# Optimization experiments

Measured on AMD Instinct MI355X. Metric: run time of the kernel, lower is better.

## Reference

```python
import jax, jax.numpy as jnp
import numpy as np

TAU = 5.0    # greybox_pars['ps'] residence time
DELTA = 1.0  # greybox_pars['Delta'] sample time


def setup_inputs() -> dict:
    key = jax.random.key(0)
    ks = jax.random.split(key, 8)
    B, T, Nx, Nu, H = 8192, 128, 3, 1, 64
    f32 = jnp.float32
    u = jax.random.normal(ks[0], (B, T, Nu), f32)
    x0 = jax.random.normal(ks[1], (B, Nx), f32)
    # fN MLP params: Dense(64, tanh) -> Dense(64, tanh) -> Dense(3)
    W1 = jax.random.normal(ks[2], (Nx + Nu, H), f32) / np.sqrt(Nx + Nu)
    b1 = jnp.zeros((H,), f32)
    W2 = jax.random.normal(ks[3], (H, H), f32) / np.sqrt(H)
    b2 = jnp.zeros((H,), f32)
    W3 = jax.random.normal(ks[4], (H, Nx), f32) / np.sqrt(H)
    b3 = jnp.zeros((Nx,), f32)
    # xuyscales
    xmean = jnp.array([1.0, 0.5, 0.3], f32)
    xstd = jnp.array([0.5, 0.2, 0.1], f32)
    umean = jnp.array([2.0], f32)
    ustd = jnp.array([0.5], f32)
    return dict(u=u, x0=x0, W1=W1, b1=b1, W2=W2, b2=b2, W3=W3, b3=b3,
                xmean=xmean, xstd=xstd, umean=umean, ustd=ustd)


def reference(u, x0, W1, b1, W2, b2, W3, b3, xmean, xstd, umean, ustd):
    def fnn(z):
        h = jnp.tanh(z @ W1 + b1)
        h = jnp.tanh(h @ W2 + b2)
        return h @ W3 + b3

    def fgreybox(x, uu):
        xp = x * xstd + xmean          # unscale state
        up = uu * ustd + umean         # unscale input
        Ca, Cb, Cc = xp[..., 0:1], xp[..., 1:2], xp[..., 2:3]
        Caf = up[..., 0:1]
        xdot = jnp.concatenate([(Caf - Ca) / TAU, -Cb / TAU, -Cc / TAU], axis=-1)
        return xdot / xstd

    def f(x, uu):
        return fgreybox(x, uu) + fnn(jnp.concatenate([x, uu], axis=-1))

    def step(x, ut):
        k1 = f(x, ut)
        k2 = f(x + DELTA * k1 / 2, ut)
        k3 = f(x + DELTA * k2 / 2, ut)
        k4 = f(x + DELTA * k3, ut)
        xplus = x + (DELTA / 6) * (k1 + 2 * k2 + 2 * k3 + k4)
        return xplus, x  # output y = current state (pre-update), as in the cell

    u_t = jnp.swapaxes(u, 0, 1)  # [T, B, Nu]
    _, ys = jax.lax.scan(step, x0, u_t)
    return jnp.swapaxes(ys, 0, 1)  # [B, T, Nx]
```

## Files before the change

### kernel.cpp

```cpp
#include <hip/hip_runtime.h>

typedef _Float16 f16x4 __attribute__((ext_vector_type(4)));
typedef _Float16 f16x8 __attribute__((ext_vector_type(8)));
typedef float    f32x4 __attribute__((ext_vector_type(4)));
typedef unsigned int u32x2 __attribute__((ext_vector_type(2)));

#if __has_builtin(__builtin_amdgcn_exp2f)
#define EXP2F __builtin_amdgcn_exp2f
#else
#define EXP2F exp2f
#endif
#if __has_builtin(__builtin_amdgcn_rcpf)
#define RCPF __builtin_amdgcn_rcpf
#else
#define RCPF(x) (1.0f/(x))
#endif

#define K2 2.8853900817779268f

static __device__ __forceinline__ float sigr(float d) {
    return RCPF(EXP2F(d) + 1.0f);
}

static __device__ __forceinline__ unsigned pkrtz(float a, float b) {
    auto t = __builtin_amdgcn_cvt_pkrtz(a, b);
    return __builtin_bit_cast(unsigned, t);
}

static __device__ __forceinline__ f32x4 mfma16(f16x4 a, f16x4 b, f32x4 c) {
#if __has_builtin(__builtin_amdgcn_mfma_f32_16x16x16f16)
    return __builtin_amdgcn_mfma_f32_16x16x16f16(a, b, c, 0, 0, 0);
#else
    f16x8 a8 = {a[0], a[1], a[2], a[3], 0, 0, 0, 0};
    f16x8 b8 = {b[0], b[1], b[2], b[3], 0, 0, 0, 0};
    return __builtin_amdgcn_mfma_f32_16x16x32_f16(a8, b8, c, 0, 0, 0);
#endif
}

extern "C" __global__ __launch_bounds__(256, 2)
void rk4_kernel(const float* __restrict__ gu,  const float* __restrict__ gx0,
                const float* __restrict__ gW1, const float* __restrict__ gb1,
                const float* __restrict__ gW2, const float* __restrict__ gb2,
                const float* __restrict__ gW3, const float* __restrict__ gb3,
                const float* __restrict__ gxm, const float* __restrict__ gxs,
                const float* __restrict__ gum, const float* __restrict__ gus,
                float* __restrict__ gout)
{
    constexpr int T = 128;
    const int tid  = threadIdx.x;
    const int lane = tid & 63;
    const int w    = tid >> 6;
    const int c    = lane & 15;
    const int g    = lane >> 4;
    const int batch = blockIdx.x * 16 + c;

    __shared__ __align__(16) _Float16 hb[2][16][72];

    f16x4 aW1;
#pragma unroll
    for (int j = 0; j < 4; ++j)
        aW1[j] = (_Float16)((g == 0) ? K2 * gW1[j * 64 + w * 16 + c] : 0.0f);

    f16x8 aW2[2];
#pragma unroll
    for (int kt = 0; kt < 2; ++kt)
#pragma unroll
        for (int j = 0; j < 8; ++j) {
            int k = kt * 32 + g * 8 + j;
            aW2[kt][j] = (_Float16)(-2.0f * K2 * gW2[k * 64 + w * 16 + c]);
        }

    f16x8 aW3[2];
#pragma unroll
    for (int kt = 0; kt < 2; ++kt)
#pragma unroll
        for (int j = 0; j < 8; ++j) {
            int k = kt * 32 + g * 8 + j;
            aW3[kt][j] = (_Float16)((c < 3) ? -2.0f * gW3[k * 3 + c] : 0.0f);
        }

    f32x4 cb1, cb2;
#pragma unroll
    for (int r = 0; r < 4; ++r) {
        int row = w * 16 + g * 4 + r;
        cb1[r] = K2 * gb1[row];
        float rs = gb2[row];
        for (int k = 0; k < 64; ++k) rs += gW2[k * 64 + row];
        cb2[r] = K2 * rs;
    }

    const float xs0 = gxs[0], xs1 = gxs[1], xs2 = gxs[2];
    const float ig0 = 1.0f / (5.0f * xs0);
    const float ig1 = 1.0f / (5.0f * xs1);
    const float ig2 = 1.0f / (5.0f * xs2);
    const float ku  = gus[0] * ig0;
    float rs3[3];
#pragma unroll
    for (int m = 0; m < 3; ++m) {
        float s = gb3[m];
        for (int k = 0; k < 64; ++k) s += gW3[k * 3 + m];
        rs3[m] = s;
    }
    f32x4 cgb;
    cgb[0] = rs3[0] + (gum[0] - gxm[0]) * ig0;
    cgb[1] = rs3[1] - gxm[1] * ig1;
    cgb[2] = rs3[2] - gxm[2] * ig2;
    cgb[3] = 0.0f;
    const float cgb0_base = cgb[0];

    float x0v = gx0[batch * 3 + 0];
    float x1v = gx0[batch * 3 + 1];
    float x2v = gx0[batch * 3 + 2];

    auto feval = [&](float e0, float e1, float e2, float ue,
                     float& o0, float& o1, float& o2) {
        unsigned z01 = 0u, z23 = 0u;
        if (g == 0) { z01 = pkrtz(e0, e1); z23 = pkrtz(e2, ue); }
        u32x2 zi = {z01, z23};
        f16x4 zb = __builtin_bit_cast(f16x4, zi);

        f32x4 d1 = mfma16(aW1, zb, cb1);
        u32x2 hw = {pkrtz(sigr(d1[0]), sigr(d1[1])),
                    pkrtz(sigr(d1[2]), sigr(d1[3]))};
        *(u32x2*)&hb[0][c][w * 16 + g * 4] = hw;
        __syncthreads();
        f16x8 hA0 = *(const f16x8*)&hb[0][c][g * 8];
        f16x8 hA1 = *(const f16x8*)&hb[0][c][32 + g * 8];

        f32x4 d2 = __builtin_amdgcn_mfma_f32_16x16x32_f16(aW2[0], hA0, cb2, 0, 0, 0);
        d2 = __builtin_amdgcn_mfma_f32_16x16x32_f16(aW2[1], hA1, d2, 0, 0, 0);
        u32x2 qw = {pkrtz(sigr(d2[0]), sigr(d2[1])),
                    pkrtz(sigr(d2[2]), sigr(d2[3]))};
        *(u32x2*)&hb[1][c][w * 16 + g * 4] = qw;
        __syncthreads();
        f16x8 hB0 = *(const f16x8*)&hb[1][c][g * 8];
        f16x8 hB1 = *(const f16x8*)&hb[1][c][32 + g * 8];

        f32x4 d3 = __builtin_amdgcn_mfma_f32_16x16x32_f16(aW3[0], hB0, cgb, 0, 0, 0);
        d3 = __builtin_amdgcn_mfma_f32_16x16x32_f16(aW3[1], hB1, d3, 0, 0, 0);

        o0 = __builtin_fmaf(-0.2f, e0, d3[0]);
        o1 = __builtin_fmaf(-0.2f, e1, d3[1]);
        o2 = __builtin_fmaf(-0.2f, e2, d3[2]);
    };

    float ucur = gu[batch * T];
    float* orow = gout + (size_t)batch * (3 * T);

    for (int t = 0; t < T; ++t) {
        if (w == 0 && g == 0) {
            orow[t * 3 + 0] = x0v;
            orow[t * 3 + 1] = x1v;
            orow[t * 3 + 2] = x2v;
        }
        float unext = gu[batch * T + ((t + 1 < T) ? t + 1 : t)];

        cgb[0] = __builtin_fmaf(ucur, ku, cgb0_base);

        float a0, a1, a2, b0, b1v, b2v, c0, c1, c2, d0, d1v, d2v;
        feval(x0v, x1v, x2v, ucur, a0, a1, a2);
        feval(x0v + 0.5f * a0, x1v + 0.5f * a1, x2v + 0.5f * a2, ucur, b0, b1v, b2v);
        feval(x0v + 0.5f * b0, x1v + 0.5f * b1v, x2v + 0.5f * b2v, ucur, c0, c1, c2);
        feval(x0v + c0, x1v + c1, x2v + c2, ucur, d0, d1v, d2v);

        x0v += (1.0f / 6.0f) * (a0 + 2.0f * b0 + 2.0f * c0 + d0);
        x1v += (1.0f / 6.0f) * (a1 + 2.0f * b1v + 2.0f * c1 + d1v);
        x2v += (1.0f / 6.0f) * (a2 + 2.0f * b2v + 2.0f * c2 + d2v);
        ucur = unext;
    }
}

extern "C" void kernel_launch(void* const* d_in, const int* in_sizes, int n_in,
                              void* d_out, int out_size, void* d_ws, size_t ws_size,
                              hipStream_t stream) {
    const float* u  = (const float*)d_in[0];
    const float* x0 = (const float*)d_in[1];
    const float* W1 = (const float*)d_in[2];
    const float* b1 = (const float*)d_in[3];
    const float* W2 = (const float*)d_in[4];
    const float* b2 = (const float*)d_in[5];
    const float* W3 = (const float*)d_in[6];
    const float* b3 = (const float*)d_in[7];
    const float* xm = (const float*)d_in[8];
    const float* xs = (const float*)d_in[9];
    const float* um = (const float*)d_in[10];
    const float* us = (const float*)d_in[11];
    rk4_kernel<<<512, 256, 0, stream>>>(u, x0, W1, b1, W2, b2, W3, b3,
                                        xm, xs, um, us, (float*)d_out);
}
```

Baseline: 224.9 us.

## Process two batch tiles per block to interleave independent MFMA chains

Each block now handles 32 batch rows as two independent 16-row tiles whose RK4 evaluations are interleaved, sharing weights and barriers. The grid is halved and launch bounds drop to one block per CU. This aims to hide MFMA and transcendental latency with instruction-level parallelism and to halve barrier count per batch row. It raises register pressure and removes cross-block occupancy as a latency-hiding source.

```diff
diff --git a/kernel.cpp b/kernel.cpp
--- a/kernel.cpp
+++ b/kernel.cpp
@@ -37,7 +37,7 @@
 #endif
 }
 
-extern "C" __global__ __launch_bounds__(256, 2)
+extern "C" __global__ __launch_bounds__(256, 1)
 void rk4_kernel(const float* __restrict__ gu,  const float* __restrict__ gx0,
                 const float* __restrict__ gW1, const float* __restrict__ gb1,
                 const float* __restrict__ gW2, const float* __restrict__ gb2,
@@ -52,9 +52,11 @@
     const int w    = tid >> 6;
     const int c    = lane & 15;
     const int g    = lane >> 4;
-    const int batch = blockIdx.x * 16 + c;
-
-    __shared__ __align__(16) _Float16 hb[2][16][72];
+    const int batchA = blockIdx.x * 32 + c;
+    const int batchB = batchA + 16;
+    const int hrow = w * 16 + g * 4;
+
+    __shared__ __align__(16) _Float16 hb[2][2][16][72];
 
     f16x4 aW1;
 #pragma unroll
@@ -82,7 +84,7 @@
     f32x4 cb1, cb2;
 #pragma unroll
     for (int r = 0; r < 4; ++r) {
-        int row = w * 16 + g * 4 + r;
+        int row = hrow + r;
         cb1[r] = K2 * gb1[row];
         float rs = gb2[row];
         for (int k = 0; k < 64; ++k) rs += gW2[k * 64 + row];
@@ -101,72 +103,107 @@
         for (int k = 0; k < 64; ++k) s += gW3[k * 3 + m];
         rs3[m] = s;
     }
-    f32x4 cgb;
-    cgb[0] = rs3[0] + (gum[0] - gxm[0]) * ig0;
-    cgb[1] = rs3[1] - gxm[1] * ig1;
-    cgb[2] = rs3[2] - gxm[2] * ig2;
-    cgb[3] = 0.0f;
-    const float cgb0_base = cgb[0];
-
-    float x0v = gx0[batch * 3 + 0];
-    float x1v = gx0[batch * 3 + 1];
-    float x2v = gx0[batch * 3 + 2];
-
-    auto feval = [&](float e0, float e1, float e2, float ue,
-                     float& o0, float& o1, float& o2) {
-        unsigned z01 = 0u, z23 = 0u;
-        if (g == 0) { z01 = pkrtz(e0, e1); z23 = pkrtz(e2, ue); }
-        u32x2 zi = {z01, z23};
-        f16x4 zb = __builtin_bit_cast(f16x4, zi);
-
-        f32x4 d1 = mfma16(aW1, zb, cb1);
-        u32x2 hw = {pkrtz(sigr(d1[0]), sigr(d1[1])),
-                    pkrtz(sigr(d1[2]), sigr(d1[3]))};
-        *(u32x2*)&hb[0][c][w * 16 + g * 4] = hw;
+    const float cgb0_base = rs3[0] + (gum[0] - gxm[0]) * ig0;
+    f32x4 cgbA, cgbB;
+    cgbA[1] = cgbB[1] = rs3[1] - gxm[1] * ig1;
+    cgbA[2] = cgbB[2] = rs3[2] - gxm[2] * ig2;
+    cgbA[3] = cgbB[3] = 0.0f;
+
+    float xA0 = gx0[batchA * 3 + 0], xA1 = gx0[batchA * 3 + 1], xA2 = gx0[batchA * 3 + 2];
+    float xB0 = gx0[batchB * 3 + 0], xB1 = gx0[batchB * 3 + 1], xB2 = gx0[batchB * 3 + 2];
+
+    auto feval2 = [&](float eA0, float eA1, float eA2, float uA,
+                      float eB0, float eB1, float eB2, float uB,
+                      float& oA0, float& oA1, float& oA2,
+                      float& oB0, float& oB1, float& oB2) {
+        unsigned zA01 = 0u, zA23 = 0u, zB01 = 0u, zB23 = 0u;
+        if (g == 0) {
+            zA01 = pkrtz(eA0, eA1); zA23 = pkrtz(eA2, uA);
+            zB01 = pkrtz(eB0, eB1); zB23 = pkrtz(eB2, uB);
+        }
+        u32x2 ziA = {zA01, zA23}, ziB = {zB01, zB23};
+        f16x4 zbA = __builtin_bit_cast(f16x4, ziA);
+        f16x4 zbB = __builtin_bit_cast(f16x4, ziB);
+
+        f32x4 d1A = mfma16(aW1, zbA, cb1);
+        f32x4 d1B = mfma16(aW1, zbB, cb1);
+        u32x2 hwA = {pkrtz(sigr(d1A[0]), sigr(d1A[1])), pkrtz(sigr(d1A[2]), sigr(d1A[3]))};
+        u32x2 hwB = {pkrtz(sigr(d1B[0]), sigr(d1B[1])), pkrtz(sigr(d1B[2]), sigr(d1B[3]))};
+        *(u32x2*)&hb[0][0][c][hrow] = hwA;
+        *(u32x2*)&hb[0][1][c][hrow] = hwB;
         __syncthreads();
-        f16x8 hA0 = *(const f16x8*)&hb[0][c][g * 8];
-        f16x8 hA1 = *(const f16x8*)&hb[0][c][32 + g * 8];
-
-        f32x4 d2 = __builtin_amdgcn_mfma_f32_16x16x32_f16(aW2[0], hA0, cb2, 0, 0, 0);
-        d2 = __builtin_amdgcn_mfma_f32_16x16x32_f16(aW2[1], hA1, d2, 0, 0, 0);
-        u32x2 qw = {pkrtz(sigr(d2[0]), sigr(d2[1])),
-                    pkrtz(sigr(d2[2]), sigr(d2[3]))};
-        *(u32x2*)&hb[1][c][w * 16 + g * 4] = qw;
+        f16x8 hA0A = *(const f16x8*)&hb[0][0][c][g * 8];
+        f16x8 hA1A = *(const f16x8*)&hb[0][0][c][32 + g * 8];
+        f16x8 hA0B = *(const f16x8*)&hb[0][1][c][g * 8];
+        f16x8 hA1B = *(const f16x8*)&hb[0][1][c][32 + g * 8];
+
+        f32x4 d2A = __builtin_amdgcn_mfma_f32_16x16x32_f16(aW2[0], hA0A, cb2, 0, 0, 0);
+        f32x4 d2B = __builtin_amdgcn_mfma_f32_16x16x32_f16(aW2[0], hA0B, cb2, 0, 0, 0);
+        d2A = __builtin_amdgcn_mfma_f32_16x16x32_f16(aW2[1], hA1A, d2A, 0, 0, 0);
+        d2B = __builtin_amdgcn_mfma_f32_16x16x32_f16(aW2[1], hA1B, d2B, 0, 0, 0);
+        u32x2 qwA = {pkrtz(sigr(d2A[0]), sigr(d2A[1])), pkrtz(sigr(d2A[2]), sigr(d2A[3]))};
+        u32x2 qwB = {pkrtz(sigr(d2B[0]), sigr(d2B[1])), pkrtz(sigr(d2B[2]), sigr(d2B[3]))};
+        *(u32x2*)&hb[1][0][c][hrow] = qwA;
+        *(u32x2*)&hb[1][1][c][hrow] = qwB;
         __syncthreads();
-        f16x8 hB0 = *(const f16x8*)&hb[1][c][g * 8];
-        f16x8 hB1 = *(const f16x8*)&hb[1][c][32 + g * 8];
-
-        f32x4 d3 = __builtin_amdgcn_mfma_f32_16x16x32_f16(aW3[0], hB0, cgb, 0, 0, 0);
-        d3 = __builtin_amdgcn_mfma_f32_16x16x32_f16(aW3[1], hB1, d3, 0, 0, 0);
-
-        o0 = __builtin_fmaf(-0.2f, e0, d3[0]);
-        o1 = __builtin_fmaf(-0.2f, e1, d3[1]);
-        o2 = __builtin_fmaf(-0.2f, e2, d3[2]);
+        f16x8 hB0A = *(const f16x8*)&hb[1][0][c][g * 8];
+        f16x8 hB1A = *(const f16x8*)&hb[1][0][c][32 + g * 8];
+        f16x8 hB0B = *(const f16x8*)&hb[1][1][c][g * 8];
+        f16x8 hB1B = *(const f16x8*)&hb[1][1][c][32 + g * 8];
+
+        f32x4 d3A = __builtin_amdgcn_mfma_f32_16x16x32_f16(aW3[0], hB0A, cgbA, 0, 0, 0);
+        f32x4 d3B = __builtin_amdgcn_mfma_f32_16x16x32_f16(aW3[0], hB0B, cgbB, 0, 0, 0);
+        d3A = __builtin_amdgcn_mfma_f32_16x16x32_f16(aW3[1], hB1A, d3A, 0, 0, 0);
+        d3B = __builtin_amdgcn_mfma_f32_16x16x32_f16(aW3[1], hB1B, d3B, 0, 0, 0);
+
+        oA0 = __builtin_fmaf(-0.2f, eA0, d3A[0]);
+        oA1 = __builtin_fmaf(-0.2f, eA1, d3A[1]);
+        oA2 = __builtin_fmaf(-0.2f, eA2, d3A[2]);
+        oB0 = __builtin_fmaf(-0.2f, eB0, d3B[0]);
+        oB1 = __builtin_fmaf(-0.2f, eB1, d3B[1]);
+        oB2 = __builtin_fmaf(-0.2f, eB2, d3B[2]);
     };
 
-    float ucur = gu[batch * T];
-    float* orow = gout + (size_t)batch * (3 * T);
+    float uA = gu[batchA * T];
+    float uB = gu[batchB * T];
+    float* orowA = gout + (size_t)batchA * (3 * T);
+    float* orowB = gout + (size_t)batchB * (3 * T);
 
     for (int t = 0; t < T; ++t) {
         if (w == 0 && g == 0) {
-            orow[t * 3 + 0] = x0v;
-            orow[t * 3 + 1] = x1v;
-            orow[t * 3 + 2] = x2v;
-        }
-        float unext = gu[batch * T + ((t + 1 < T) ? t + 1 : t)];
-
-        cgb[0] = __builtin_fmaf(ucur, ku, cgb0_base);
-
-        float a0, a1, a2, b0, b1v, b2v, c0, c1, c2, d0, d1v, d2v;
-        feval(x0v, x1v, x2v, ucur, a0, a1, a2);
-        feval(x0v + 0.5f * a0, x1v + 0.5f * a1, x2v + 0.5f * a2, ucur, b0, b1v, b2v);
-        feval(x0v + 0.5f * b0, x1v + 0.5f * b1v, x2v + 0.5f * b2v, ucur, c0, c1, c2);
-        feval(x0v + c0, x1v + c1, x2v + c2, ucur, d0, d1v, d2v);
-
-        x0v += (1.0f / 6.0f) * (a0 + 2.0f * b0 + 2.0f * c0 + d0);
-        x1v += (1.0f / 6.0f) * (a1 + 2.0f * b1v + 2.0f * c1 + d1v);
-        x2v += (1.0f / 6.0f) * (a2 + 2.0f * b2v + 2.0f * c2 + d2v);
-        ucur = unext;
+            orowA[t * 3 + 0] = xA0; orowA[t * 3 + 1] = xA1; orowA[t * 3 + 2] = xA2;
+            orowB[t * 3 + 0] = xB0; orowB[t * 3 + 1] = xB1; orowB[t * 3 + 2] = xB2;
+        }
+        int tn = (t + 1 < T) ? t + 1 : t;
+        float unA = gu[batchA * T + tn];
+        float unB = gu[batchB * T + tn];
+
+        cgbA[0] = __builtin_fmaf(uA, ku, cgb0_base);
+        cgbB[0] = __builtin_fmaf(uB, ku, cgb0_base);
+
+        float aA0, aA1, aA2, bA0, bA1, bA2, cA0, cA1, cA2, dA0, dA1, dA2;
+        float aB0, aB1, aB2, bB0, bB1, bB2, cB0, cB1, cB2, dB0, dB1, dB2;
+
+        feval2(xA0, xA1, xA2, uA,  xB0, xB1, xB2, uB,
+               aA0, aA1, aA2, aB0, aB1, aB2);
+        feval2(xA0 + 0.5f * aA0, xA1 + 0.5f * aA1, xA2 + 0.5f * aA2, uA,
+               xB0 + 0.5f * aB0, xB1 + 0.5f * aB1, xB2 + 0.5f * aB2, uB,
+               bA0, bA1, bA2, bB0, bB1, bB2);
+        feval2(xA0 + 0.5f * bA0, xA1 + 0.5f * bA1, xA2 + 0.5f * bA2, uA,
+               xB0 + 0.5f * bB0, xB1 + 0.5f * bB1, xB2 + 0.5f * bB2, uB,
+               cA0, cA1, cA2, cB0, cB1, cB2);
+        feval2(xA0 + cA0, xA1 + cA1, xA2 + cA2, uA,
+               xB0 + cB0, xB1 + cB1, xB2 + cB2, uB,
+               dA0, dA1, dA2, dB0, dB1, dB2);
+
+        xA0 += (1.0f / 6.0f) * (aA0 + 2.0f * bA0 + 2.0f * cA0 + dA0);
+        xA1 += (1.0f / 6.0f) * (aA1 + 2.0f * bA1 + 2.0f * cA1 + dA1);
+        xA2 += (1.0f / 6.0f) * (aA2 + 2.0f * bA2 + 2.0f * cA2 + dA2);
+        xB0 += (1.0f / 6.0f) * (aB0 + 2.0f * bB0 + 2.0f * cB0 + dB0);
+        xB1 += (1.0f / 6.0f) * (aB1 + 2.0f * bB1 + 2.0f * cB1 + dB1);
+        xB2 += (1.0f / 6.0f) * (aB2 + 2.0f * bB2 + 2.0f * cB2 + dB2);
+        uA = unA;
+        uB = unB;
     }
 }
 
@@ -185,6 +222,6 @@
     const float* xs = (const float*)d_in[9];
     const float* um = (const float*)d_in[10];
     const float* us = (const float*)d_in[11];
-    rk4_kernel<<<512, 256, 0, stream>>>(u, x0, W1, b1, W2, b2, W3, b3,
+    rk4_kernel<<<256, 256, 0, stream>>>(u, x0, W1, b1, W2, b2, W3, b3,
                                         xm, xs, um, us, (float*)d_out);
 }
```

Measured after the change: 316.4 us. +40.7%, slower.

## Compute each 16-batch MLP in a single wavefront without LDS or barriers

Applied to the files above, without the earlier changes.

Instead of splitting the 64 hidden units across four wavefronts that exchange activations through shared memory with two barriers per evaluation, one wavefront now computes all four 16-row tiles itself. It uses 16x16x16 MFMAs whose output register layout feeds straight into the next layer's B operand. This removes the LDS round trips and __syncthreads from the serial RK4 dependency chain. The cost is four times more MFMA and sigmoid work per wave and more registers for weights. With only 512 single-wave blocks, the GPU runs far fewer waves at once to hide latency.

```diff
diff --git a/kernel.cpp b/kernel.cpp
--- a/kernel.cpp
+++ b/kernel.cpp
@@ -37,7 +37,7 @@
 #endif
 }
 
-extern "C" __global__ __launch_bounds__(256, 2)
+extern "C" __global__ __launch_bounds__(64, 1)
 void rk4_kernel(const float* __restrict__ gu,  const float* __restrict__ gx0,
                 const float* __restrict__ gW1, const float* __restrict__ gb1,
                 const float* __restrict__ gW2, const float* __restrict__ gb2,
@@ -47,47 +47,47 @@
                 float* __restrict__ gout)
 {
     constexpr int T = 128;
-    const int tid  = threadIdx.x;
-    const int lane = tid & 63;
-    const int w    = tid >> 6;
+    const int lane = threadIdx.x & 63;
     const int c    = lane & 15;
     const int g    = lane >> 4;
     const int batch = blockIdx.x * 16 + c;
 
-    __shared__ __align__(16) _Float16 hb[2][16][72];
-
-    f16x4 aW1;
-#pragma unroll
-    for (int j = 0; j < 4; ++j)
-        aW1[j] = (_Float16)((g == 0) ? K2 * gW1[j * 64 + w * 16 + c] : 0.0f);
-
-    f16x8 aW2[2];
-#pragma unroll
-    for (int kt = 0; kt < 2; ++kt)
-#pragma unroll
-        for (int j = 0; j < 8; ++j) {
-            int k = kt * 32 + g * 8 + j;
-            aW2[kt][j] = (_Float16)(-2.0f * K2 * gW2[k * 64 + w * 16 + c]);
-        }
-
-    f16x8 aW3[2];
-#pragma unroll
-    for (int kt = 0; kt < 2; ++kt)
-#pragma unroll
-        for (int j = 0; j < 8; ++j) {
-            int k = kt * 32 + g * 8 + j;
-            aW3[kt][j] = (_Float16)((c < 3) ? -2.0f * gW3[k * 3 + c] : 0.0f);
-        }
-
-    f32x4 cb1, cb2;
-#pragma unroll
-    for (int r = 0; r < 4; ++r) {
-        int row = w * 16 + g * 4 + r;
-        cb1[r] = K2 * gb1[row];
-        float rs = gb2[row];
-        for (int k = 0; k < 64; ++k) rs += gW2[k * 64 + row];
-        cb2[r] = K2 * rs;
-    }
+    f16x4 aW1[4];
+#pragma unroll
+    for (int mt = 0; mt < 4; ++mt)
+#pragma unroll
+        for (int j = 0; j < 4; ++j)
+            aW1[mt][j] = (_Float16)((g == 0) ? K2 * gW1[j * 64 + mt * 16 + c] : 0.0f);
+
+    f16x4 aW2[4][4];
+#pragma unroll
+    for (int mt = 0; mt < 4; ++mt)
+#pragma unroll
+        for (int ks = 0; ks < 4; ++ks)
+#pragma unroll
+            for (int j = 0; j < 4; ++j)
+                aW2[mt][ks][j] =
+                    (_Float16)(-2.0f * K2 * gW2[(ks * 16 + g * 4 + j) * 64 + mt * 16 + c]);
+
+    f16x4 aW3[4];
+#pragma unroll
+    for (int ks = 0; ks < 4; ++ks)
+#pragma unroll
+        for (int j = 0; j < 4; ++j)
+            aW3[ks][j] =
+                (_Float16)((c < 3) ? -2.0f * gW3[(ks * 16 + g * 4 + j) * 3 + c] : 0.0f);
+
+    f32x4 cb1[4], cb2[4];
+#pragma unroll
+    for (int mt = 0; mt < 4; ++mt)
+#pragma unroll
+        for (int r = 0; r < 4; ++r) {
+            int row = mt * 16 + g * 4 + r;
+            cb1[mt][r] = K2 * gb1[row];
+            float rs = gb2[row];
+            for (int k = 0; k < 64; ++k) rs += gW2[k * 64 + row];
+            cb2[mt][r] = K2 * rs;
+        }
 
     const float xs0 = gxs[0], xs1 = gxs[1], xs2 = gxs[2];
     const float ig0 = 1.0f / (5.0f * xs0);
@@ -101,12 +101,11 @@
         for (int k = 0; k < 64; ++k) s += gW3[k * 3 + m];
         rs3[m] = s;
     }
+    const float cgb0_base = rs3[0] + (gum[0] - gxm[0]) * ig0;
     f32x4 cgb;
-    cgb[0] = rs3[0] + (gum[0] - gxm[0]) * ig0;
-    cgb[1] = rs3[1] - gxm[1] * ig1;
-    cgb[2] = rs3[2] - gxm[2] * ig2;
+    cgb[1] = (g == 0) ? (rs3[1] - gxm[1] * ig1) : 0.0f;
+    cgb[2] = (g == 0) ? (rs3[2] - gxm[2] * ig2) : 0.0f;
     cgb[3] = 0.0f;
-    const float cgb0_base = cgb[0];
 
     float x0v = gx0[batch * 3 + 0];
     float x1v = gx0[batch * 3 + 1];
@@ -119,25 +118,51 @@
         u32x2 zi = {z01, z23};
         f16x4 zb = __builtin_bit_cast(f16x4, zi);
 
-        f32x4 d1 = mfma16(aW1, zb, cb1);
-        u32x2 hw = {pkrtz(sigr(d1[0]), sigr(d1[1])),
-                    pkrtz(sigr(d1[2]), sigr(d1[3]))};
-        *(u32x2*)&hb[0][c][w * 16 + g * 4] = hw;
-        __syncthreads();
-        f16x8 hA0 = *(const f16x8*)&hb[0][c][g * 8];
-        f16x8 hA1 = *(const f16x8*)&hb[0][c][32 + g * 8];
-
-        f32x4 d2 = __builtin_amdgcn_mfma_f32_16x16x32_f16(aW2[0], hA0, cb2, 0, 0, 0);
-        d2 = __builtin_amdgcn_mfma_f32_16x16x32_f16(aW2[1], hA1, d2, 0, 0, 0);
-        u32x2 qw = {pkrtz(sigr(d2[0]), sigr(d2[1])),
-                    pkrtz(sigr(d2[2]), sigr(d2[3]))};
-        *(u32x2*)&hb[1][c][w * 16 + g * 4] = qw;
-        __syncthreads();
-        f16x8 hB0 = *(const f16x8*)&hb[1][c][g * 8];
-        f16x8 hB1 = *(const f16x8*)&hb[1][c][32 + g * 8];
-
-        f32x4 d3 = __builtin_amdgcn_mfma_f32_16x16x32_f16(aW3[0], hB0, cgb, 0, 0, 0);
-        d3 = __builtin_amdgcn_mfma_f32_16x16x32_f16(aW3[1], hB1, d3, 0, 0, 0);
+        f32x4 d1_0 = mfma16(aW1[0], zb, cb1[0]);
+        f32x4 d1_1 = mfma16(aW1[1], zb, cb1[1]);
+        f32x4 d1_2 = mfma16(aW1[2], zb, cb1[2]);
+        f32x4 d1_3 = mfma16(aW1[3], zb, cb1[3]);
+
+        f16x4 pk1[4];
+        {
+            u32x2 t0 = {pkrtz(sigr(d1_0[0]), sigr(d1_0[1])), pkrtz(sigr(d1_0[2]), sigr(d1_0[3]))};
+            u32x2 t1 = {pkrtz(sigr(d1_1[0]), sigr(d1_1[1])), pkrtz(sigr(d1_1[2]), sigr(d1_1[3]))};
+            u32x2 t2 = {pkrtz(sigr(d1_2[0]), sigr(d1_2[1])), pkrtz(sigr(d1_2[2]), sigr(d1_2[3]))};
+            u32x2 t3 = {pkrtz(sigr(d1_3[0]), sigr(d1_3[1])), pkrtz(sigr(d1_3[2]), sigr(d1_3[3]))};
+            pk1[0] = __builtin_bit_cast(f16x4, t0);
+            pk1[1] = __builtin_bit_cast(f16x4, t1);
+            pk1[2] = __builtin_bit_cast(f16x4, t2);
+            pk1[3] = __builtin_bit_cast(f16x4, t3);
+        }
+
+        f32x4 d2_0 = mfma16(aW2[0][0], pk1[0], cb2[0]);
+        f32x4 d2_1 = mfma16(aW2[1][0], pk1[0], cb2[1]);
+        f32x4 d2_2 = mfma16(aW2[2][0], pk1[0], cb2[2]);
+        f32x4 d2_3 = mfma16(aW2[3][0], pk1[0], cb2[3]);
+#pragma unroll
+        for (int ks = 1; ks < 4; ++ks) {
+            d2_0 = mfma16(aW2[0][ks], pk1[ks], d2_0);
+            d2_1 = mfma16(aW2[1][ks], pk1[ks], d2_1);
+            d2_2 = mfma16(aW2[2][ks], pk1[ks], d2_2);
+            d2_3 = mfma16(aW2[3][ks], pk1[ks], d2_3);
+        }
+
+        f16x4 pk2[4];
+        {
+            u32x2 t0 = {pkrtz(sigr(d2_0[0]), sigr(d2_0[1])), pkrtz(sigr(d2_0[2]), sigr(d2_0[3]))};
+            u32x2 t1 = {pkrtz(sigr(d2_1[0]), sigr(d2_1[1])), pkrtz(sigr(d2_1[2]), sigr(d2_1[3]))};
+            u32x2 t2 = {pkrtz(sigr(d2_2[0]), sigr(d2_2[1])), pkrtz(sigr(d2_2[2]), sigr(d2_2[3]))};
+            u32x2 t3 = {pkrtz(sigr(d2_3[0]), sigr(d2_3[1])), pkrtz(sigr(d2_3[2]), sigr(d2_3[3]))};
+            pk2[0] = __builtin_bit_cast(f16x4, t0);
+            pk2[1] = __builtin_bit_cast(f16x4, t1);
+            pk2[2] = __builtin_bit_cast(f16x4, t2);
+            pk2[3] = __builtin_bit_cast(f16x4, t3);
+        }
+
+        f32x4 d3 = mfma16(aW3[0], pk2[0], cgb);
+        d3 = mfma16(aW3[1], pk2[1], d3);
+        d3 = mfma16(aW3[2], pk2[2], d3);
+        d3 = mfma16(aW3[3], pk2[3], d3);
 
         o0 = __builtin_fmaf(-0.2f, e0, d3[0]);
         o1 = __builtin_fmaf(-0.2f, e1, d3[1]);
@@ -148,14 +173,14 @@
     float* orow = gout + (size_t)batch * (3 * T);
 
     for (int t = 0; t < T; ++t) {
-        if (w == 0 && g == 0) {
+        if (g == 0) {
             orow[t * 3 + 0] = x0v;
             orow[t * 3 + 1] = x1v;
             orow[t * 3 + 2] = x2v;
         }
         float unext = gu[batch * T + ((t + 1 < T) ? t + 1 : t)];
 
-        cgb[0] = __builtin_fmaf(ucur, ku, cgb0_base);
+        cgb[0] = (g == 0) ? __builtin_fmaf(ucur, ku, cgb0_base) : 0.0f;
 
         float a0, a1, a2, b0, b1v, b2v, c0, c1, c2, d0, d1v, d2v;
         feval(x0v, x1v, x2v, ucur, a0, a1, a2);
@@ -185,6 +210,6 @@
     const float* xs = (const float*)d_in[9];
     const float* um = (const float*)d_in[10];
     const float* us = (const float*)d_in[11];
-    rk4_kernel<<<512, 256, 0, stream>>>(u, x0, W1, b1, W2, b2, W3, b3,
-                                        xm, xs, um, us, (float*)d_out);
-}
+    rk4_kernel<<<512, 64, 0, stream>>>(u, x0, W1, b1, W2, b2, W3, b3,
+                                       xm, xs, um, us, (float*)d_out);
+}
```

New measurement: 315.6 us. 40.4% more time.

## Interleave two batch tiles per block in a staggered three-stage MLP pipeline

Applied to the files above, without the earlier changes.

Each block now runs two 16-sample tiles in two groups of four waves. The MLP evaluation is split into three stages, and the groups are offset so that while one group runs a stage the other runs a different one. Two dependent phases share each barrier, which halves the barrier count per evaluation, and a custom barrier waits only on LDS. The block grows to 512 threads and the grid halves, which may change occupancy and register pressure and adds scheduling complexity.

```diff
diff --git a/kernel.cpp b/kernel.cpp
--- a/kernel.cpp
+++ b/kernel.cpp
@@ -37,7 +37,13 @@
 #endif
 }
 
-extern "C" __global__ __launch_bounds__(256, 2)
+static __device__ __forceinline__ void barrier_lds() {
+    asm volatile("s_waitcnt lgkmcnt(0)\n\ts_barrier" ::: "memory");
+}
+
+template<int N> struct ic { static constexpr int v = N; };
+
+extern "C" __global__ __launch_bounds__(512, 2)
 void rk4_kernel(const float* __restrict__ gu,  const float* __restrict__ gx0,
                 const float* __restrict__ gW1, const float* __restrict__ gb1,
                 const float* __restrict__ gW2, const float* __restrict__ gb2,
@@ -49,17 +55,21 @@
     constexpr int T = 128;
     const int tid  = threadIdx.x;
     const int lane = tid & 63;
-    const int w    = tid >> 6;
+    const int wv   = tid >> 6;
+    const int wt   = wv >> 2;
+    const int ws   = wv & 3;
     const int c    = lane & 15;
     const int g    = lane >> 4;
-    const int batch = blockIdx.x * 16 + c;
-
-    __shared__ __align__(16) _Float16 hb[2][16][72];
+    const int batch = blockIdx.x * 32 + wt * 16 + c;
+    const int hrow  = ws * 16 + g * 4;
+
+    __shared__ __align__(16) _Float16 h1[2][16][72];
+    __shared__ __align__(16) _Float16 h2[2][16][72];
 
     f16x4 aW1;
 #pragma unroll
     for (int j = 0; j < 4; ++j)
-        aW1[j] = (_Float16)((g == 0) ? K2 * gW1[j * 64 + w * 16 + c] : 0.0f);
+        aW1[j] = (_Float16)((g == 0) ? K2 * gW1[j * 64 + ws * 16 + c] : 0.0f);
 
     f16x8 aW2[2];
 #pragma unroll
@@ -67,7 +77,7 @@
 #pragma unroll
         for (int j = 0; j < 8; ++j) {
             int k = kt * 32 + g * 8 + j;
-            aW2[kt][j] = (_Float16)(-2.0f * K2 * gW2[k * 64 + w * 16 + c]);
+            aW2[kt][j] = (_Float16)(-2.0f * K2 * gW2[k * 64 + ws * 16 + c]);
         }
 
     f16x8 aW3[2];
@@ -82,7 +92,7 @@
     f32x4 cb1, cb2;
 #pragma unroll
     for (int r = 0; r < 4; ++r) {
-        int row = w * 16 + g * 4 + r;
+        int row = hrow + r;
         cb1[r] = K2 * gb1[row];
         float rs = gb2[row];
         for (int k = 0; k < 64; ++k) rs += gW2[k * 64 + row];
@@ -101,73 +111,112 @@
         for (int k = 0; k < 64; ++k) s += gW3[k * 3 + m];
         rs3[m] = s;
     }
+    const float cgb0_base = rs3[0] + (gum[0] - gxm[0]) * ig0;
     f32x4 cgb;
-    cgb[0] = rs3[0] + (gum[0] - gxm[0]) * ig0;
     cgb[1] = rs3[1] - gxm[1] * ig1;
     cgb[2] = rs3[2] - gxm[2] * ig2;
     cgb[3] = 0.0f;
-    const float cgb0_base = cgb[0];
 
     float x0v = gx0[batch * 3 + 0];
     float x1v = gx0[batch * 3 + 1];
     float x2v = gx0[batch * 3 + 2];
-
-    auto feval = [&](float e0, float e1, float e2, float ue,
-                     float& o0, float& o1, float& o2) {
+    float e0 = x0v, e1 = x1v, e2 = x2v;
+    float ks0 = 0.0f, ks1 = 0.0f, ks2 = 0.0f;
+    float u  = gu[batch * T];
+    float un = u;
+    cgb[0] = __builtin_fmaf(u, ku, cgb0_base);
+    int t = 0;
+    float* orow = gout + (size_t)batch * (3 * T);
+
+    auto S0 = [&]() {
         unsigned z01 = 0u, z23 = 0u;
-        if (g == 0) { z01 = pkrtz(e0, e1); z23 = pkrtz(e2, ue); }
+        if (g == 0) { z01 = pkrtz(e0, e1); z23 = pkrtz(e2, u); }
         u32x2 zi = {z01, z23};
         f16x4 zb = __builtin_bit_cast(f16x4, zi);
-
         f32x4 d1 = mfma16(aW1, zb, cb1);
         u32x2 hw = {pkrtz(sigr(d1[0]), sigr(d1[1])),
                     pkrtz(sigr(d1[2]), sigr(d1[3]))};
-        *(u32x2*)&hb[0][c][w * 16 + g * 4] = hw;
-        __syncthreads();
-        f16x8 hA0 = *(const f16x8*)&hb[0][c][g * 8];
-        f16x8 hA1 = *(const f16x8*)&hb[0][c][32 + g * 8];
-
-        f32x4 d2 = __builtin_amdgcn_mfma_f32_16x16x32_f16(aW2[0], hA0, cb2, 0, 0, 0);
-        d2 = __builtin_amdgcn_mfma_f32_16x16x32_f16(aW2[1], hA1, d2, 0, 0, 0);
+        *(u32x2*)&h1[wt][c][hrow] = hw;
+    };
+    auto S1 = [&]() {
+        f16x8 a0 = *(const f16x8*)&h1[wt][c][g * 8];
+        f16x8 a1 = *(const f16x8*)&h1[wt][c][32 + g * 8];
+        f32x4 d2 = __builtin_amdgcn_mfma_f32_16x16x32_f16(aW2[0], a0, cb2, 0, 0, 0);
+        d2 = __builtin_amdgcn_mfma_f32_16x16x32_f16(aW2[1], a1, d2, 0, 0, 0);
         u32x2 qw = {pkrtz(sigr(d2[0]), sigr(d2[1])),
                     pkrtz(sigr(d2[2]), sigr(d2[3]))};
-        *(u32x2*)&hb[1][c][w * 16 + g * 4] = qw;
-        __syncthreads();
-        f16x8 hB0 = *(const f16x8*)&hb[1][c][g * 8];
-        f16x8 hB1 = *(const f16x8*)&hb[1][c][32 + g * 8];
-
-        f32x4 d3 = __builtin_amdgcn_mfma_f32_16x16x32_f16(aW3[0], hB0, cgb, 0, 0, 0);
-        d3 = __builtin_amdgcn_mfma_f32_16x16x32_f16(aW3[1], hB1, d3, 0, 0, 0);
-
-        o0 = __builtin_fmaf(-0.2f, e0, d3[0]);
-        o1 = __builtin_fmaf(-0.2f, e1, d3[1]);
-        o2 = __builtin_fmaf(-0.2f, e2, d3[2]);
+        *(u32x2*)&h2[wt][c][hrow] = qw;
     };
-
-    float ucur = gu[batch * T];
-    float* orow = gout + (size_t)batch * (3 * T);
-
-    for (int t = 0; t < T; ++t) {
-        if (w == 0 && g == 0) {
-            orow[t * 3 + 0] = x0v;
-            orow[t * 3 + 1] = x1v;
-            orow[t * 3 + 2] = x2v;
+    auto S2 = [&](auto stc) {
+        constexpr int ST = decltype(stc)::v;
+        f16x8 b0 = *(const f16x8*)&h2[wt][c][g * 8];
+        f16x8 b1 = *(const f16x8*)&h2[wt][c][32 + g * 8];
+        f32x4 d3 = __builtin_amdgcn_mfma_f32_16x16x32_f16(aW3[0], b0, cgb, 0, 0, 0);
+        d3 = __builtin_amdgcn_mfma_f32_16x16x32_f16(aW3[1], b1, d3, 0, 0, 0);
+        float o0 = __builtin_fmaf(-0.2f, e0, d3[0]);
+        float o1 = __builtin_fmaf(-0.2f, e1, d3[1]);
+        float o2 = __builtin_fmaf(-0.2f, e2, d3[2]);
+        if constexpr (ST == 0) {
+            ks0 = o0; ks1 = o1; ks2 = o2;
+            e0 = __builtin_fmaf(0.5f, o0, x0v);
+            e1 = __builtin_fmaf(0.5f, o1, x1v);
+            e2 = __builtin_fmaf(0.5f, o2, x2v);
+            un = gu[batch * T + ((t + 1 < T) ? t + 1 : T - 1)];
+        } else if constexpr (ST == 1) {
+            ks0 = __builtin_fmaf(2.0f, o0, ks0);
+            ks1 = __builtin_fmaf(2.0f, o1, ks1);
+            ks2 = __builtin_fmaf(2.0f, o2, ks2);
+            e0 = __builtin_fmaf(0.5f, o0, x0v);
+            e1 = __builtin_fmaf(0.5f, o1, x1v);
+            e2 = __builtin_fmaf(0.5f, o2, x2v);
+        } else if constexpr (ST == 2) {
+            ks0 = __builtin_fmaf(2.0f, o0, ks0);
+            ks1 = __builtin_fmaf(2.0f, o1, ks1);
+            ks2 = __builtin_fmaf(2.0f, o2, ks2);
+            e0 = x0v + o0;
+            e1 = x1v + o1;
+            e2 = x2v + o2;
+        } else {
+            x0v += (1.0f / 6.0f) * (ks0 + o0);
+            x1v += (1.0f / 6.0f) * (ks1 + o1);
+            x2v += (1.0f / 6.0f) * (ks2 + o2);
+            int tn = t + 1;
+            if (tn < T && ws == 0 && g == 0) {
+                orow[tn * 3 + 0] = x0v;
+                orow[tn * 3 + 1] = x1v;
+                orow[tn * 3 + 2] = x2v;
+            }
+            t = tn;
+            u = un;
+            cgb[0] = __builtin_fmaf(u, ku, cgb0_base);
+            e0 = x0v; e1 = x1v; e2 = x2v;
         }
-        float unext = gu[batch * T + ((t + 1 < T) ? t + 1 : t)];
-
-        cgb[0] = __builtin_fmaf(ucur, ku, cgb0_base);
-
-        float a0, a1, a2, b0, b1v, b2v, c0, c1, c2, d0, d1v, d2v;
-        feval(x0v, x1v, x2v, ucur, a0, a1, a2);
-        feval(x0v + 0.5f * a0, x1v + 0.5f * a1, x2v + 0.5f * a2, ucur, b0, b1v, b2v);
-        feval(x0v + 0.5f * b0, x1v + 0.5f * b1v, x2v + 0.5f * b2v, ucur, c0, c1, c2);
-        feval(x0v + c0, x1v + c1, x2v + c2, ucur, d0, d1v, d2v);
-
-        x0v += (1.0f / 6.0f) * (a0 + 2.0f * b0 + 2.0f * c0 + d0);
-        x1v += (1.0f / 6.0f) * (a1 + 2.0f * b1v + 2.0f * c1 + d1v);
-        x2v += (1.0f / 6.0f) * (a2 + 2.0f * b2v + 2.0f * c2 + d2v);
-        ucur = unext;
-    }
+    };
+
+    if (ws == 0 && g == 0) {
+        orow[0] = x0v; orow[1] = x1v; orow[2] = x2v;
+    }
+    if (wt == 0) { S0(); }
+    barrier_lds();
+    if (wt == 0) { S1(); } else { S0(); }
+    barrier_lds();
+
+#define PAIR(S)                                                   \
+    if (wt == 0) { S2(ic<S>{}); S0(); } else { S1(); }            \
+    barrier_lds();                                                \
+    if (wt == 0) { S1(); } else { S2(ic<S>{}); S0(); }            \
+    barrier_lds();
+
+#pragma unroll 1
+    for (int it = 0; it < 127; ++it) {
+        PAIR(0) PAIR(1) PAIR(2) PAIR(3)
+    }
+    PAIR(0) PAIR(1) PAIR(2)
+
+    if (wt == 0) { S2(ic<3>{}); } else { S1(); }
+    barrier_lds();
+    if (wt == 1) { S2(ic<3>{}); }
+#undef PAIR
 }
 
 extern "C" void kernel_launch(void* const* d_in, const int* in_sizes, int n_in,
@@ -185,6 +234,6 @@
     const float* xs = (const float*)d_in[9];
     const float* um = (const float*)d_in[10];
     const float* us = (const float*)d_in[11];
-    rk4_kernel<<<512, 256, 0, stream>>>(u, x0, W1, b1, W2, b2, W3, b3,
+    rk4_kernel<<<256, 512, 0, stream>>>(u, x0, W1, b1, W2, b2, W3, b3,
                                         xm, xs, um, us, (float*)d_out);
 }
```

Result: slower. 292.5 us (+30.1%).
